# Kernel tuning notes

Measured on AMD Instinct MI355X. Metric: run time of the kernel, lower is better.

Reference implementation:

```python
import jax, jax.numpy as jnp
import numpy as np

TREE_DEPTH = 4
N_LEAVES = 2 ** TREE_DEPTH      # 16
N_INTERNAL = 2 ** TREE_DEPTH - 1  # 15
TEMP = 1.0
EPS = 1e-5


def _build_paths(depth):
    nl = 2 ** depth
    pi = np.zeros((nl, depth), np.int32)
    pd = np.zeros((nl, depth), np.float32)
    for leaf in range(nl):
        node = 0
        for d in range(depth):
            pi[leaf, d] = node
            bit = (leaf >> (depth - 1 - d)) & 1
            pd[leaf, d] = 1.0 - bit
            node = 2 * node + 1 + bit
    return jnp.asarray(pi), jnp.asarray(pd)

PATH_IDX, PATH_DIR = _build_paths(TREE_DEPTH)


def setup_inputs() -> dict:
    key = jax.random.key(0)
    k0, k1, k2, k3 = jax.random.split(key, 4)
    B, S, D, O, T = 4, 2048, 1024, 512, 16
    x = jax.random.normal(k0, (B, S, D), jnp.float32)
    decision_weights = 0.1 * jax.random.normal(k1, (T, N_INTERNAL, D), jnp.float32)
    decision_biases = jnp.zeros((T, N_INTERNAL), jnp.float32)
    xavier = float(np.sqrt(2.0 / (N_LEAVES + O)))
    leaf_outputs = xavier * jax.random.normal(k2, (T, N_LEAVES, O), jnp.float32)
    gate_w = 0.02 * jax.random.normal(k3, (D, T), jnp.float32)
    gate_b = jnp.zeros((T,), jnp.float32)
    node_temp_logits = jnp.zeros((T, N_INTERNAL), jnp.float32)
    ln_gamma = jnp.ones((O,), jnp.float32)
    ln_beta = jnp.zeros((O,), jnp.float32)
    return dict(x=x, decision_weights=decision_weights, decision_biases=decision_biases,
                leaf_outputs=leaf_outputs, gate_w=gate_w, gate_b=gate_b,
                node_temp_logits=node_temp_logits, ln_gamma=ln_gamma, ln_beta=ln_beta)


def reference(x, decision_weights, decision_biases, leaf_outputs,
              gate_w, gate_b, node_temp_logits, ln_gamma, ln_beta):
    # decision logits: (B,S,T,N)
    logits = jnp.einsum('bsd,tnd->bstn', x, decision_weights) + decision_biases
    # per-node learnable temperature (softplus(0.5413) ~= 1)
    node_temps = TEMP * jax.nn.softplus(node_temp_logits + 0.5413)
    decisions = jax.nn.sigmoid(logits / node_temps)
    # gather decisions along each root->leaf path: (B,S,T,L,depth)
    relevant = decisions[..., PATH_IDX]
    probs_per_level = PATH_DIR * relevant + (1.0 - PATH_DIR) * (1.0 - relevant)
    leaf_probs = jnp.prod(probs_per_level, axis=-1)  # (B,S,T,L)
    per_tree = jnp.einsum('bstl,tlo->bsto', leaf_probs, leaf_outputs)
    gate = jax.nn.softmax(x @ gate_w + gate_b, axis=-1)  # (B,S,T)
    out = jnp.einsum('bsto,bst->bso', per_tree, gate)
    # LayerNorm over last dim
    mu = jnp.mean(out, axis=-1, keepdims=True)
    var = jnp.var(out, axis=-1, keepdims=True)
    return (out - mu) / jnp.sqrt(var + EPS) * ln_gamma + ln_beta
```

## Files before the change

### kernel.cpp

```cpp
#include <hip/hip_runtime.h>
#include <math.h>

#define TOK 8192
#define DD  1024
#define OO  512
#define NC  256

#define WC4_HI 0
#define WC4_LO (512*1024)
#define LO4_HI (1024*1024)
#define LO4_LO (1280*1024)
#define PAR_B  (1536*1024)

typedef __attribute__((ext_vector_type(8))) short short8;
typedef __attribute__((ext_vector_type(4))) float f32x4;

#define MFMA16(a,b,c) __builtin_amdgcn_mfma_f32_16x16x32_bf16((a),(b),(c),0,0,0)

__device__ __forceinline__ ushort f2bh(float f) {
  union { float f; unsigned u; } v; v.f = f;
  unsigned r = v.u + 0x7fffu + ((v.u >> 16) & 1u);
  return (ushort)(r >> 16);
}
__device__ __forceinline__ float bh2f(ushort h) {
  union { unsigned u; float f; } v; v.u = ((unsigned)h) << 16; return v.f;
}
__device__ __forceinline__ void split2(float f, ushort& h, ushort& l) {
  h = f2bh(f);
  l = f2bh(f - bh2f(h));
}

__global__ __launch_bounds__(256) void k_prep(
    const float* __restrict__ dw, const float* __restrict__ db,
    const float* __restrict__ lo_in, const float* __restrict__ gw,
    const float* __restrict__ ntl, char* __restrict__ ws) {
  const int bid = blockIdx.x, tid = threadIdx.x;
  if (bid < 16) {
    __shared__ char pt[65536];
    const int n0 = (bid & 3) * 64;
    const int k0 = (bid >> 2) * 256;
    const int kl4 = (tid & 63) << 2;
#pragma unroll
    for (int i = 0; i < 16; ++i) {
      const int row = (tid >> 6) + 4 * i;
      const int n = n0 + row;
      float v[4];
      if (n < 240) {
        const float4 t4 = *(const float4*)&dw[(size_t)n * DD + k0 + kl4];
        v[0] = t4.x; v[1] = t4.y; v[2] = t4.z; v[3] = t4.w;
      } else {
        const int t = n - 240;
#pragma unroll
        for (int c = 0; c < 4; ++c) v[c] = gw[(size_t)(k0 + kl4 + c) * 16 + t];
      }
      ushort4 h, l;
      split2(v[0], h.x, l.x); split2(v[1], h.y, l.y);
      split2(v[2], h.z, l.z); split2(v[3], h.w, l.w);
      const int u = kl4 >> 3, half = (kl4 >> 2) & 1;
      const int boff = row * 512 + ((u ^ (row & 31)) << 4) + half * 8;
      *(ushort4*)(pt + boff) = h;
      *(ushort4*)(pt + 32768 + boff) = l;
    }
    __syncthreads();
#pragma unroll
    for (int j = 0; j < 8; ++j) {
      const int u = tid + 256 * j;
      const int c = u & 63;
      const int kk = u >> 6;
      const int src = c * 512 + ((kk ^ (c & 31)) << 4);
      const size_t dst = ((size_t)((k0 >> 3) + kk) * 256 + n0 + c) * 16;
      *(short8*)(ws + WC4_HI + dst) = *(const short8*)(pt + src);
      *(short8*)(ws + WC4_LO + dst) = *(const short8*)(pt + 32768 + src);
    }
  } else if (bid < 80) {
    const int idx  = (bid - 16) * 256 + tid;
    const int k8   = idx >> 9;
    const int ocol = idx & 511;
    float v[8];
#pragma unroll
    for (int c = 0; c < 8; ++c) v[c] = lo_in[(size_t)(k8 * 8 + c) * OO + ocol];
    short8 h, l;
#pragma unroll
    for (int e = 0; e < 8; ++e) {
      ushort hh, ll; split2(v[e], hh, ll);
      h[e] = (short)hh; l[e] = (short)ll;
    }
    const size_t o16 = ((size_t)k8 * 512 + ocol) * 16;
    *(short8*)(ws + LO4_HI + o16) = h;
    *(short8*)(ws + LO4_LO + o16) = l;
  } else {
    if (tid < 240) {
      float v = ntl[tid] + 0.5413f;
      float sp = (v > 20.f) ? v : log1pf(expf(v));
      float* par = (float*)(ws + PAR_B);
      par[tid]       = db[tid];
      par[240 + tid] = 1.0f / sp;
    }
  }
}

#define XSB(b)  ((b) * 16384)
#define WF_HI   32768
#define WF_LO   49152
#define SM_SZ   65536

__global__ __launch_bounds__(1024) void k_fused(
    const float* __restrict__ x, const char* __restrict__ ws,
    const float* __restrict__ gate_b, const float* __restrict__ gamma,
    const float* __restrict__ beta, float* __restrict__ out) {
  __shared__ __align__(16) char sm[SM_SZ];

  const char* wc4_hi = ws + WC4_HI;
  const char* wc4_lo = ws + WC4_LO;
  const char* lo4_hi = ws + LO4_HI;
  const char* lo4_lo = ws + LO4_LO;
  const float* par   = (const float*)(ws + PAR_B);

  const int tid  = threadIdx.x;
  const int wv   = tid >> 6;
  const int lane = tid & 63;
  const int l15  = lane & 15;
  const int kgrp = lane >> 4;
  const int m0   = blockIdx.x * 32;

  f32x4 acc00 = {0,0,0,0}, acc10 = {0,0,0,0};
  short8 ah0, ah1, al0, al1;
  short8 b1h[4], b1l[4];
  float4 px;

  const int xm = tid >> 5;
  const int xk = (tid & 31) << 2;

  auto xload = [&](int CH) {
    px = *(const float4*)&x[(size_t)(m0 + xm) * DD + CH * 128 + xk];
  };
  auto xstore = [&](int BUF) {
    ushort4 h, l;
    split2(px.x, h.x, l.x); split2(px.y, h.y, l.y);
    split2(px.z, h.z, l.z); split2(px.w, h.w, l.w);
    const int off = (xm * 256 + xk * 2) ^ ((xm & 15) << 4);
    *(ushort4*)(sm + XSB(BUF) + off) = h;
    *(ushort4*)(sm + XSB(BUF) + 8192 + off) = l;
  };
#define LOADB1(F, S) do {                                               \
    const int Fc = (F) < 31 ? (F) : 31;                                 \
    const size_t o = ((size_t)(Fc * 4 + kgrp) * 256 + wv * 16 + l15) * 16; \
    b1h[S] = *(const short8*)(wc4_hi + o);                              \
    b1l[S] = *(const short8*)(wc4_lo + o);                              \
  } while (0)
  auto afrag = [&](int CB, int KS) {
    const int k0 = KS * 64 + kgrp * 16;
    const int a0 = (l15 * 256 + k0) ^ (l15 << 4);
    const int a1 = ((16 + l15) * 256 + k0) ^ (l15 << 4);
    ah0 = *(const short8*)(sm + XSB(CB) + a0);
    al0 = *(const short8*)(sm + XSB(CB) + 8192 + a0);
    ah1 = *(const short8*)(sm + XSB(CB) + a1);
    al1 = *(const short8*)(sm + XSB(CB) + 8192 + a1);
  };
#define MFMASTEP(S) do {                                                \
    acc00 = MFMA16(ah0, b1h[S], acc00);                                 \
    acc00 = MFMA16(ah0, b1l[S], acc00);                                 \
    acc00 = MFMA16(al0, b1h[S], acc00);                                 \
    acc10 = MFMA16(ah1, b1h[S], acc10);                                 \
    acc10 = MFMA16(ah1, b1l[S], acc10);                                 \
    acc10 = MFMA16(al1, b1h[S], acc10);                                 \
  } while (0)

  xload(0);
  xstore(0);
  LOADB1(0, 0);
  LOADB1(1, 1);

  for (int ch = 0; ch < 8; ++ch) {
    __syncthreads();
    const int cb = ch & 1;
    if (ch < 7) xload(ch + 1);
    const int f = ch * 4;
    LOADB1(f + 2, 2); afrag(cb, 0); MFMASTEP(0);
    LOADB1(f + 3, 3); afrag(cb, 1); MFMASTEP(1);
    LOADB1(f + 4, 0); afrag(cb, 2); MFMASTEP(2);
    LOADB1(f + 5, 1); afrag(cb, 3); MFMASTEP(3);
    if (ch < 7) xstore(cb ^ 1);
  }
  __syncthreads();

  {
    float* actp = (float*)sm;
    const int col = wv * 16 + l15;
#pragma unroll
    for (int r = 0; r < 4; ++r) {
      actp[(kgrp * 4 + r) * 256 + col]      = acc00[r];
      actp[(16 + kgrp * 4 + r) * 256 + col] = acc10[r];
    }
  }
  __syncthreads();

  short8 c2h[3][2], c2l[3][2];
#define LOADB2(F, S) do {                                               \
    const size_t base = ((size_t)((F) * 4 + kgrp) * 512) * 16;          \
    _Pragma("unroll")                                                   \
    for (int t = 0; t < 2; ++t) {                                       \
      const size_t o = base + (size_t)(wv * 32 + t * 16 + l15) * 16;    \
      c2h[S][t] = *(const short8*)(lo4_hi + o);                         \
      c2l[S][t] = *(const short8*)(lo4_lo + o);                         \
    }                                                                   \
  } while (0)
  LOADB2(0, 0);
  LOADB2(1, 1);

  if (tid < 512) {
    const float* actp = (const float*)sm;
    const int token = tid >> 4;
    const int tr    = tid & 15;
    const float* arow_p = actp + token * 256;

    float dec[15];
#pragma unroll
    for (int i = 0; i < 15; ++i) {
      const int ci = tr * 15 + i;
      const float z = (arow_p[ci] + par[ci]) * par[240 + ci];
      dec[i] = 1.f / (1.f + expf(-z));
    }
    float gl = arow_p[240 + tr] + gate_b[tr];
    float gmax = gl;
#pragma unroll
    for (int msk = 8; msk >= 1; msk >>= 1) gmax = fmaxf(gmax, __shfl_xor(gmax, msk, 16));
    const float ge = expf(gl - gmax);
    float gsum = ge;
#pragma unroll
    for (int msk = 8; msk >= 1; msk >>= 1) gsum += __shfl_xor(gsum, msk, 16);
    const float gate = ge / gsum;

    float lp[16];
#pragma unroll
    for (int l = 0; l < 16; ++l) {
      float p = gate;
      int node = 0;
#pragma unroll
      for (int d = 0; d < 4; ++d) {
        const int bit = (l >> (3 - d)) & 1;
        p *= bit ? (1.f - dec[node]) : dec[node];
        node = 2 * node + 1 + bit;
      }
      lp[l] = p;
    }
    short8 h0, h1, l0, l1;
#pragma unroll
    for (int e = 0; e < 8; ++e) {
      ushort hh, ll;
      split2(lp[e], hh, ll);     h0[e] = (short)hh; l0[e] = (short)ll;
      split2(lp[8 + e], hh, ll); h1[e] = (short)hh; l1[e] = (short)ll;
    }
    const int b0 = (token * 512 + tr * 32) ^ ((token & 15) << 4);
    const int b1 = (token * 512 + tr * 32 + 16) ^ ((token & 15) << 4);
    *(short8*)(sm + WF_HI + b0) = h0;
    *(short8*)(sm + WF_HI + b1) = h1;
    *(short8*)(sm + WF_LO + b0) = l0;
    *(short8*)(sm + WF_LO + b1) = l1;
  }
  __syncthreads();

  f32x4 ac0[2], ac1[2];
#pragma unroll
  for (int t = 0; t < 2; ++t) { ac0[t] = (f32x4){0,0,0,0}; ac1[t] = (f32x4){0,0,0,0}; }
  short8 wah0, wah1, wal0, wal1;
  auto wafrag = [&](int FC) {
    const int k0 = FC * 64 + kgrp * 16;
    const int a0 = (l15 * 512 + k0) ^ (l15 << 4);
    const int a1 = ((16 + l15) * 512 + k0) ^ (l15 << 4);
    wah0 = *(const short8*)(sm + WF_HI + a0);
    wal0 = *(const short8*)(sm + WF_LO + a0);
    wah1 = *(const short8*)(sm + WF_HI + a1);
    wal1 = *(const short8*)(sm + WF_LO + a1);
  };
#define MFMA2STEP(S) do {                                               \
    _Pragma("unroll")                                                   \
    for (int t = 0; t < 2; ++t) {                                       \
      ac0[t] = MFMA16(wah0, c2h[S][t], ac0[t]);                         \
      ac0[t] = MFMA16(wah0, c2l[S][t], ac0[t]);                         \
      ac0[t] = MFMA16(wal0, c2h[S][t], ac0[t]);                         \
      ac1[t] = MFMA16(wah1, c2h[S][t], ac1[t]);                         \
      ac1[t] = MFMA16(wah1, c2l[S][t], ac1[t]);                         \
      ac1[t] = MFMA16(wal1, c2h[S][t], ac1[t]);                         \
    }                                                                   \
  } while (0)

  LOADB2(2, 2); wafrag(0); MFMA2STEP(0);
  LOADB2(3, 0); wafrag(1); MFMA2STEP(1);
  LOADB2(4, 1); wafrag(2); MFMA2STEP(2);
  LOADB2(5, 2); wafrag(3); MFMA2STEP(0);
  LOADB2(6, 0); wafrag(4); MFMA2STEP(1);
  LOADB2(7, 1); wafrag(5); MFMA2STEP(2);
  wafrag(6); MFMA2STEP(0);
  wafrag(7); MFMA2STEP(1);

  float* ps = (float*)sm;
#pragma unroll
  for (int mi = 0; mi < 2; ++mi)
#pragma unroll
    for (int r = 0; r < 4; ++r) {
      float s = 0.f, q = 0.f;
#pragma unroll
      for (int t = 0; t < 2; ++t) {
        const float v = (mi == 0) ? ac0[t][r] : ac1[t][r];
        s += v; q += v * v;
      }
#pragma unroll
      for (int msk = 8; msk >= 1; msk >>= 1) {
        s += __shfl_xor(s, msk, 16);
        q += __shfl_xor(q, msk, 16);
      }
      if (l15 == 0) {
        const int row = mi * 16 + kgrp * 4 + r;
        ps[(row * 16 + wv) * 2 + 0] = s;
        ps[(row * 16 + wv) * 2 + 1] = q;
      }
    }
  __syncthreads();

#pragma unroll
  for (int mi = 0; mi < 2; ++mi)
#pragma unroll
    for (int r = 0; r < 4; ++r) {
      const int row = mi * 16 + kgrp * 4 + r;
      float S = 0.f, Q = 0.f;
#pragma unroll
      for (int p = 0; p < 16; ++p) {
        S += ps[(row * 16 + p) * 2 + 0];
        Q += ps[(row * 16 + p) * 2 + 1];
      }
      const float mu  = S * (1.f / 512.f);
      const float var = Q * (1.f / 512.f) - mu * mu;
      const float rs  = rsqrtf(var + 1e-5f);
#pragma unroll
      for (int t = 0; t < 2; ++t) {
        const int col = wv * 32 + t * 16 + l15;
        const float v = (mi == 0) ? ac0[t][r] : ac1[t][r];
        out[(size_t)(m0 + row) * OO + col] = (v - mu) * rs * gamma[col] + beta[col];
      }
    }
}

extern "C" void kernel_launch(void* const* d_in, const int* in_sizes, int n_in,
                              void* d_out, int out_size, void* d_ws, size_t ws_size,
                              hipStream_t stream) {
  const float* x   = (const float*)d_in[0];
  const float* dw  = (const float*)d_in[1];
  const float* db  = (const float*)d_in[2];
  const float* lo  = (const float*)d_in[3];
  const float* gw  = (const float*)d_in[4];
  const float* gb  = (const float*)d_in[5];
  const float* ntl = (const float*)d_in[6];
  const float* g   = (const float*)d_in[7];
  const float* b   = (const float*)d_in[8];
  char* ws   = (char*)d_ws;
  float* out = (float*)d_out;

  k_prep<<<81, 256, 0, stream>>>(dw, db, lo, gw, ntl, ws);
  k_fused<<<256, 1024, 0, stream>>>(x, ws, gb, g, b, out);
}
```

Before: 124.1 us.

## Preload all x chunks into registers upfront and widen prep kernel blocks

The fused kernel now issues all eight x chunk loads at the start and splits them to bf16 hi/lo in registers, instead of loading one chunk per iteration inside the GEMM loop. This hides global-load latency behind the whole first stage, at the cost of extra VGPRs (16 ushort4 held live) in a 1024-thread block, which could cause spills. The prep kernel is also relaunched with 1024-thread blocks and fewer blocks, with its loops rescaled to match. The main loop is fully unrolled.

New measurement: 123.9 us. Within noise of the previous version (-0.2%).

```diff
diff --git a/kernel.cpp b/kernel.cpp
--- a/kernel.cpp
+++ b/kernel.cpp
@@ -30,7 +30,7 @@
   l = f2bh(f - bh2f(h));
 }
 
-__global__ __launch_bounds__(256) void k_prep(
+__global__ __launch_bounds__(1024) void k_prep(
     const float* __restrict__ dw, const float* __restrict__ db,
     const float* __restrict__ lo_in, const float* __restrict__ gw,
     const float* __restrict__ ntl, char* __restrict__ ws) {
@@ -41,8 +41,8 @@
     const int k0 = (bid >> 2) * 256;
     const int kl4 = (tid & 63) << 2;
 #pragma unroll
-    for (int i = 0; i < 16; ++i) {
-      const int row = (tid >> 6) + 4 * i;
+    for (int i = 0; i < 4; ++i) {
+      const int row = (tid >> 6) + 16 * i;
       const int n = n0 + row;
       float v[4];
       if (n < 240) {
@@ -63,8 +63,8 @@
     }
     __syncthreads();
 #pragma unroll
-    for (int j = 0; j < 8; ++j) {
-      const int u = tid + 256 * j;
+    for (int j = 0; j < 2; ++j) {
+      const int u = tid + 1024 * j;
       const int c = u & 63;
       const int kk = u >> 6;
       const int src = c * 512 + ((kk ^ (c & 31)) << 4);
@@ -72,8 +72,8 @@
       *(short8*)(ws + WC4_HI + dst) = *(const short8*)(pt + src);
       *(short8*)(ws + WC4_LO + dst) = *(const short8*)(pt + 32768 + src);
     }
-  } else if (bid < 80) {
-    const int idx  = (bid - 16) * 256 + tid;
+  } else if (bid < 32) {
+    const int idx  = (bid - 16) * 1024 + tid;
     const int k8   = idx >> 9;
     const int ocol = idx & 511;
     float v[8];
@@ -123,25 +123,33 @@
   const int kgrp = lane >> 4;
   const int m0   = blockIdx.x * 32;
 
+  const int xm = tid >> 5;
+  const int xk = (tid & 31) << 2;
+
+  ushort4 pxh[8], pxl[8];
+  {
+    float4 t[8];
+#pragma unroll
+    for (int ch = 0; ch < 8; ++ch)
+      t[ch] = *(const float4*)&x[(size_t)(m0 + xm) * DD + ch * 128 + xk];
+#pragma unroll
+    for (int ch = 0; ch < 8; ++ch) {
+      split2(t[ch].x, pxh[ch].x, pxl[ch].x);
+      split2(t[ch].y, pxh[ch].y, pxl[ch].y);
+      split2(t[ch].z, pxh[ch].z, pxl[ch].z);
+      split2(t[ch].w, pxh[ch].w, pxl[ch].w);
+    }
+  }
+
   f32x4 acc00 = {0,0,0,0}, acc10 = {0,0,0,0};
   short8 ah0, ah1, al0, al1;
   short8 b1h[4], b1l[4];
-  float4 px;
-
-  const int xm = tid >> 5;
-  const int xk = (tid & 31) << 2;
-
-  auto xload = [&](int CH) {
-    px = *(const float4*)&x[(size_t)(m0 + xm) * DD + CH * 128 + xk];
-  };
-  auto xstore = [&](int BUF) {
-    ushort4 h, l;
-    split2(px.x, h.x, l.x); split2(px.y, h.y, l.y);
-    split2(px.z, h.z, l.z); split2(px.w, h.w, l.w);
-    const int off = (xm * 256 + xk * 2) ^ ((xm & 15) << 4);
-    *(ushort4*)(sm + XSB(BUF) + off) = h;
-    *(ushort4*)(sm + XSB(BUF) + 8192 + off) = l;
-  };
+
+#define XSTORE(CH, BUF) do {                                            \
+    const int off = (xm * 256 + xk * 2) ^ ((xm & 15) << 4);             \
+    *(ushort4*)(sm + XSB(BUF) + off) = pxh[CH];                         \
+    *(ushort4*)(sm + XSB(BUF) + 8192 + off) = pxl[CH];                  \
+  } while (0)
 #define LOADB1(F, S) do {                                               \
     const int Fc = (F) < 31 ? (F) : 31;                                 \
     const size_t o = ((size_t)(Fc * 4 + kgrp) * 256 + wv * 16 + l15) * 16; \
@@ -166,21 +174,20 @@
     acc10 = MFMA16(al1, b1h[S], acc10);                                 \
   } while (0)
 
-  xload(0);
-  xstore(0);
   LOADB1(0, 0);
   LOADB1(1, 1);
-
+  XSTORE(0, 0);
+
+#pragma unroll
   for (int ch = 0; ch < 8; ++ch) {
     __syncthreads();
     const int cb = ch & 1;
-    if (ch < 7) xload(ch + 1);
     const int f = ch * 4;
     LOADB1(f + 2, 2); afrag(cb, 0); MFMASTEP(0);
     LOADB1(f + 3, 3); afrag(cb, 1); MFMASTEP(1);
     LOADB1(f + 4, 0); afrag(cb, 2); MFMASTEP(2);
     LOADB1(f + 5, 1); afrag(cb, 3); MFMASTEP(3);
-    if (ch < 7) xstore(cb ^ 1);
+    if (ch < 7) XSTORE(ch + 1, cb ^ 1);
   }
   __syncthreads();
 
@@ -356,6 +363,6 @@
   char* ws   = (char*)d_ws;
   float* out = (float*)d_out;
 
-  k_prep<<<81, 256, 0, stream>>>(dw, db, lo, gw, ntl, ws);
+  k_prep<<<33, 1024, 0, stream>>>(dw, db, lo, gw, ntl, ws);
   k_fused<<<256, 1024, 0, stream>>>(x, ws, gb, g, b, out);
 }
```

## Stagger per-block K-chunk order to spread weight reads; widen prep blocks

Applied to the files above, without the earlier changes.

Each fused block now walks the K chunks and the second-GEMM leaf chunks in a rotated order chosen from its block index, so concurrent blocks read different parts of the shared weight arrays instead of all hitting the same addresses together. The prefetch clamp is dropped because indices now wrap modulo 32, and the main loop is fully unrolled. The prep kernel is reshaped to 1024-thread blocks, so it launches fewer blocks. The accumulation order changes per block, which gives slightly different rounding, and the unrolled loop may raise register pressure.

Measured after the change: 119.6 us. 3.7% less time.

```diff
diff --git a/kernel.cpp b/kernel.cpp
--- a/kernel.cpp
+++ b/kernel.cpp
@@ -30,7 +30,7 @@
   l = f2bh(f - bh2f(h));
 }
 
-__global__ __launch_bounds__(256) void k_prep(
+__global__ __launch_bounds__(1024) void k_prep(
     const float* __restrict__ dw, const float* __restrict__ db,
     const float* __restrict__ lo_in, const float* __restrict__ gw,
     const float* __restrict__ ntl, char* __restrict__ ws) {
@@ -41,8 +41,8 @@
     const int k0 = (bid >> 2) * 256;
     const int kl4 = (tid & 63) << 2;
 #pragma unroll
-    for (int i = 0; i < 16; ++i) {
-      const int row = (tid >> 6) + 4 * i;
+    for (int i = 0; i < 4; ++i) {
+      const int row = (tid >> 6) + 16 * i;
       const int n = n0 + row;
       float v[4];
       if (n < 240) {
@@ -63,8 +63,8 @@
     }
     __syncthreads();
 #pragma unroll
-    for (int j = 0; j < 8; ++j) {
-      const int u = tid + 256 * j;
+    for (int j = 0; j < 2; ++j) {
+      const int u = tid + 1024 * j;
       const int c = u & 63;
       const int kk = u >> 6;
       const int src = c * 512 + ((kk ^ (c & 31)) << 4);
@@ -72,8 +72,8 @@
       *(short8*)(ws + WC4_HI + dst) = *(const short8*)(pt + src);
       *(short8*)(ws + WC4_LO + dst) = *(const short8*)(pt + 32768 + src);
     }
-  } else if (bid < 80) {
-    const int idx  = (bid - 16) * 256 + tid;
+  } else if (bid < 32) {
+    const int idx  = (bid - 16) * 1024 + tid;
     const int k8   = idx >> 9;
     const int ocol = idx & 511;
     float v[8];
@@ -121,15 +121,23 @@
   const int lane = tid & 63;
   const int l15  = lane & 15;
   const int kgrp = lane >> 4;
-  const int m0   = blockIdx.x * 32;
+  const int bid  = blockIdx.x;
+  const int m0   = bid * 32;
+
+  const int rot = (bid >> 3) & 7;
+  const int r2  = (bid >> 6) & 3;
+
+  auto CHUNK = [&](int it) { return (it + rot) & 7; };
+  auto KSLOT = [&](int p)  { return (p + r2) & 3; };
+  auto FQ    = [&](int q)  { q &= 31; return CHUNK(q >> 2) * 4 + KSLOT(q & 3); };
+
+  const int xm = tid >> 5;
+  const int xk = (tid & 31) << 2;
 
   f32x4 acc00 = {0,0,0,0}, acc10 = {0,0,0,0};
   short8 ah0, ah1, al0, al1;
   short8 b1h[4], b1l[4];
   float4 px;
-
-  const int xm = tid >> 5;
-  const int xk = (tid & 31) << 2;
 
   auto xload = [&](int CH) {
     px = *(const float4*)&x[(size_t)(m0 + xm) * DD + CH * 128 + xk];
@@ -143,8 +151,7 @@
     *(ushort4*)(sm + XSB(BUF) + 8192 + off) = l;
   };
 #define LOADB1(F, S) do {                                               \
-    const int Fc = (F) < 31 ? (F) : 31;                                 \
-    const size_t o = ((size_t)(Fc * 4 + kgrp) * 256 + wv * 16 + l15) * 16; \
+    const size_t o = ((size_t)((F) * 4 + kgrp) * 256 + wv * 16 + l15) * 16; \
     b1h[S] = *(const short8*)(wc4_hi + o);                              \
     b1l[S] = *(const short8*)(wc4_lo + o);                              \
   } while (0)
@@ -166,21 +173,22 @@
     acc10 = MFMA16(al1, b1h[S], acc10);                                 \
   } while (0)
 
-  xload(0);
+  xload(CHUNK(0));
   xstore(0);
-  LOADB1(0, 0);
-  LOADB1(1, 1);
-
-  for (int ch = 0; ch < 8; ++ch) {
+  LOADB1(FQ(0), 0);
+  LOADB1(FQ(1), 1);
+
+#pragma unroll
+  for (int it = 0; it < 8; ++it) {
     __syncthreads();
-    const int cb = ch & 1;
-    if (ch < 7) xload(ch + 1);
-    const int f = ch * 4;
-    LOADB1(f + 2, 2); afrag(cb, 0); MFMASTEP(0);
-    LOADB1(f + 3, 3); afrag(cb, 1); MFMASTEP(1);
-    LOADB1(f + 4, 0); afrag(cb, 2); MFMASTEP(2);
-    LOADB1(f + 5, 1); afrag(cb, 3); MFMASTEP(3);
-    if (ch < 7) xstore(cb ^ 1);
+    const int cb = it & 1;
+    if (it < 7) xload(CHUNK(it + 1));
+    const int q = it * 4;
+    LOADB1(FQ(q + 2), 2); afrag(cb, KSLOT(0)); MFMASTEP(0);
+    LOADB1(FQ(q + 3), 3); afrag(cb, KSLOT(1)); MFMASTEP(1);
+    LOADB1(FQ(q + 4), 0); afrag(cb, KSLOT(2)); MFMASTEP(2);
+    LOADB1(FQ(q + 5), 1); afrag(cb, KSLOT(3)); MFMASTEP(3);
+    if (it < 7) xstore(cb ^ 1);
   }
   __syncthreads();
 
@@ -205,8 +213,9 @@
       c2l[S][t] = *(const short8*)(lo4_lo + o);                         \
     }                                                                   \
   } while (0)
-  LOADB2(0, 0);
-  LOADB2(1, 1);
+  auto F2 = [&](int s) { return (s + rot) & 7; };
+  LOADB2(F2(0), 0);
+  LOADB2(F2(1), 1);
 
   if (tid < 512) {
     const float* actp = (const float*)sm;
@@ -285,14 +294,14 @@
     }                                                                   \
   } while (0)
 
-  LOADB2(2, 2); wafrag(0); MFMA2STEP(0);
-  LOADB2(3, 0); wafrag(1); MFMA2STEP(1);
-  LOADB2(4, 1); wafrag(2); MFMA2STEP(2);
-  LOADB2(5, 2); wafrag(3); MFMA2STEP(0);
-  LOADB2(6, 0); wafrag(4); MFMA2STEP(1);
-  LOADB2(7, 1); wafrag(5); MFMA2STEP(2);
-  wafrag(6); MFMA2STEP(0);
-  wafrag(7); MFMA2STEP(1);
+  LOADB2(F2(2), 2); wafrag(F2(0)); MFMA2STEP(0);
+  LOADB2(F2(3), 0); wafrag(F2(1)); MFMA2STEP(1);
+  LOADB2(F2(4), 1); wafrag(F2(2)); MFMA2STEP(2);
+  LOADB2(F2(5), 2); wafrag(F2(3)); MFMA2STEP(0);
+  LOADB2(F2(6), 0); wafrag(F2(4)); MFMA2STEP(1);
+  LOADB2(F2(7), 1); wafrag(F2(5)); MFMA2STEP(2);
+  wafrag(F2(6)); MFMA2STEP(0);
+  wafrag(F2(7)); MFMA2STEP(1);
 
   float* ps = (float*)sm;
 #pragma unroll
@@ -356,6 +365,6 @@
   char* ws   = (char*)d_ws;
   float* out = (float*)d_out;
 
-  k_prep<<<81, 256, 0, stream>>>(dw, db, lo, gw, ntl, ws);
+  k_prep<<<33, 1024, 0, stream>>>(dw, db, lo, gw, ntl, ws);
   k_fused<<<256, 1024, 0, stream>>>(x, ws, gb, g, b, out);
 }
```
